# Kernel optimization log

Hardware: AMD Instinct MI355X
Metric: run time of the kernel (lower is better)

The kernel has to match this reference:

```python
import jax, jax.numpy as jnp
import numpy as np

B, S, I, H = 32, 1024, 512, 512


def setup_inputs() -> dict:
    key = jax.random.key(0)
    ks = jax.random.split(key, 5)
    scale_ih = 1.0 / np.sqrt(I)
    scale_hh = 1.0 / np.sqrt(H)
    return {
        "x": jax.random.normal(ks[0], (B, S, I), dtype=jnp.float32),
        "W_ih": jax.random.normal(ks[1], (4 * H, I), dtype=jnp.float32) * scale_ih,
        "W_hh": jax.random.normal(ks[2], (4 * H, H), dtype=jnp.float32) * scale_hh,
        "b_ih": jax.random.normal(ks[3], (4 * H,), dtype=jnp.float32) * scale_hh,
        "b_hh": jax.random.normal(ks[4], (4 * H,), dtype=jnp.float32) * scale_hh,
        "h0": jnp.zeros((B, H), dtype=jnp.float32),
        "c0": jnp.zeros((B, H), dtype=jnp.float32),
    }


def reference(x, W_ih, W_hh, b_ih, b_hh, h0, c0):
    # Precompute input contribution for all timesteps: [B, S, 4H]
    x_gates = jnp.einsum('bsi,gi->bsg', x, W_ih) + b_ih + b_hh

    def step(carry, xg_t):
        h, c = carry
        gates = xg_t + h @ W_hh.T  # [B, 4H]
        i_g, f_g, g_g, o_g = jnp.split(gates, 4, axis=-1)
        i_g = jax.nn.sigmoid(i_g)
        f_g = jax.nn.sigmoid(f_g)
        g_g = jnp.tanh(g_g)
        o_g = jax.nn.sigmoid(o_g)
        c_new = f_g * c + i_g * g_g
        h_new = o_g * jnp.tanh(c_new)
        return (h_new, c_new), h_new

    # scan over time: [S, B, 4H]
    (h_n, c_n), ys = jax.lax.scan(step, (h0, c0), jnp.swapaxes(x_gates, 0, 1))
    output = jnp.swapaxes(ys, 0, 1)  # [B, S, H]
    return output, h_n, c_n
```

## Files before the change

### kernel.cpp

```cpp
#include <hip/hip_runtime.h>
#include <stdint.h>


typedef __attribute__((ext_vector_type(8))) short bf16x8;
typedef __attribute__((ext_vector_type(4))) float f32x4;

__device__ __forceinline__ unsigned short f2bf(float f) {
  union { float f; unsigned u; } v; v.f = f;
  unsigned r = (v.u + 0x7fffu + ((v.u >> 16) & 1u)) >> 16;
  return (unsigned short)r;
}
__device__ __forceinline__ float bf2f(unsigned short h) {
  union { unsigned u; float f; } v; v.u = ((unsigned)h) << 16;
  return v.f;
}

__global__ __launch_bounds__(256) void cvt_bf16(const float* __restrict__ in,
                                                unsigned short* __restrict__ out, int n) {
  int i = (blockIdx.x * 256 + threadIdx.x) * 4;
  if (i >= n) return;
  float4 v = *(const float4*)(in + i);
  ushort4 o;
  o.x = f2bf(v.x); o.y = f2bf(v.y); o.z = f2bf(v.z); o.w = f2bf(v.w);
  *(ushort4*)(out + i) = o;
}

__global__ __launch_bounds__(256) void gemm_xg(const unsigned short* __restrict__ A,
                                               const unsigned short* __restrict__ Bw,
                                               const float* __restrict__ b_ih,
                                               const float* __restrict__ b_hh,
                                               unsigned short* __restrict__ xg) {
  __shared__ unsigned short Asub[128][32];
  __shared__ unsigned short Bsub[128][32];
  const int tid = threadIdx.x;
  const int mb = blockIdx.x >> 4;
  const int nb = blockIdx.x & 15;
  const int wv = tid >> 6, ln = tid & 63;
  const int wr = wv >> 1, wc = wv & 1;
  const int lrow = tid >> 1;
  const int lseg = (tid & 1) * 16;

  const unsigned short* Ag = A + (size_t)(mb * 128 + lrow) * 512 + lseg;
  const unsigned short* Bg = Bw + (size_t)(nb * 128 + lrow) * 512 + lseg;

  f32x4 acc[4][4] = {};
  const int frow = ln & 15;
  const int kq = (ln >> 4) * 8;

  for (int k0 = 0; k0 < 512; k0 += 32) {
    uint4 a0 = *(const uint4*)(Ag + k0);
    uint4 a1 = *(const uint4*)(Ag + k0 + 8);
    uint4 b0 = *(const uint4*)(Bg + k0);
    uint4 b1 = *(const uint4*)(Bg + k0 + 8);
    __syncthreads();
    *(uint4*)&Asub[lrow][lseg]     = a0;
    *(uint4*)&Asub[lrow][lseg + 8] = a1;
    *(uint4*)&Bsub[lrow][lseg]     = b0;
    *(uint4*)&Bsub[lrow][lseg + 8] = b1;
    __syncthreads();
    bf16x8 af[4], bfr[4];
#pragma unroll
    for (int mi = 0; mi < 4; ++mi)
      af[mi] = *(const bf16x8*)&Asub[wr * 64 + mi * 16 + frow][kq];
#pragma unroll
    for (int ni = 0; ni < 4; ++ni)
      bfr[ni] = *(const bf16x8*)&Bsub[wc * 64 + ni * 16 + frow][kq];
#pragma unroll
    for (int mi = 0; mi < 4; ++mi)
#pragma unroll
      for (int ni = 0; ni < 4; ++ni)
        acc[mi][ni] = __builtin_amdgcn_mfma_f32_16x16x32_bf16(af[mi], bfr[ni], acc[mi][ni], 0, 0, 0);
  }

  const int col0 = nb * 128 + wc * 64 + frow;
  float bias[4];
#pragma unroll
  for (int ni = 0; ni < 4; ++ni)
    bias[ni] = b_ih[col0 + ni * 16] + b_hh[col0 + ni * 16];

#pragma unroll
  for (int mi = 0; mi < 4; ++mi) {
    const int m0 = mb * 128 + wr * 64 + mi * 16 + (ln >> 4) * 4;
#pragma unroll
    for (int ni = 0; ni < 4; ++ni) {
#pragma unroll
      for (int rr = 0; rr < 4; ++rr) {
        float v = acc[mi][ni][rr] + bias[ni];
        xg[(size_t)(m0 + rr) * 2048 + col0 + ni * 16] = f2bf(v);
      }
    }
  }
}

__global__ __launch_bounds__(512, 1) void lstm_rec(const unsigned short* __restrict__ xg,
                                                   const float* __restrict__ W_hh,
                                                   const float* __restrict__ h0,
                                                   const float* __restrict__ c0,
                                                   float* __restrict__ out,
                                                   float* __restrict__ hn,
                                                   float* __restrict__ cn,
                                                   float* h_buf,
                                                   unsigned int* cnt) {
  __shared__ float h_lds[2048];
  __shared__ float scratch[2048];
  __shared__ float gates_lds[64 * 5];
  __shared__ float c_lds[64];

  const int tid = threadIdx.x;
  const int g = blockIdx.x >> 5;
  const int w = blockIdx.x & 31;
  const int gb0 = g * 4;
  const int kc = tid >> 6;
  const int r = tid & 63;
  const int grow = (r >> 4) * 512 + w * 16 + (r & 15);
  const int kcb = kc * 64;
  unsigned int* my_cnt = cnt + g * 64;

  float W[64];
  {
    const float* wp = W_hh + (size_t)grow * 512 + kcb;
#pragma unroll
    for (int i = 0; i < 64; i += 4) {
      float4 v = *(const float4*)(wp + i);
      W[i] = v.x; W[i + 1] = v.y; W[i + 2] = v.z; W[i + 3] = v.w;
    }
  }
#pragma unroll
  for (int i = 0; i < 64; ++i) asm volatile("" : "+v"(W[i]));

  {
    *(float4*)&h_lds[tid * 4] = *(const float4*)(h0 + gb0 * 512 + tid * 4);
    if (tid < 64) {
      int jj = tid & 15, bb = tid >> 4;
      c_lds[bb * 16 + jj] = c0[(gb0 + bb) * 512 + w * 16 + jj];
    }
  }
  __syncthreads();

  const int rr = tid & 63, bb2 = tid >> 6;
  const int grow_r = (rr >> 4) * 512 + w * 16 + (rr & 15);

  for (int t = 0; t < 1024; ++t) {
    float xg_v = 0.f;
    if (tid < 256)
      xg_v = bf2f(xg[(size_t)((gb0 + bb2) * 1024 + t) * 2048 + grow_r]);

    float acc0 = 0.f, acc1 = 0.f, acc2 = 0.f, acc3 = 0.f;
#pragma unroll
    for (int i = 0; i < 64; i += 4) {
      float4 ha = *(const float4*)&h_lds[kcb + i];
      float4 hb = *(const float4*)&h_lds[512 + kcb + i];
      float4 hc = *(const float4*)&h_lds[1024 + kcb + i];
      float4 hd = *(const float4*)&h_lds[1536 + kcb + i];
      acc0 = fmaf(W[i], ha.x, acc0); acc0 = fmaf(W[i + 1], ha.y, acc0);
      acc0 = fmaf(W[i + 2], ha.z, acc0); acc0 = fmaf(W[i + 3], ha.w, acc0);
      acc1 = fmaf(W[i], hb.x, acc1); acc1 = fmaf(W[i + 1], hb.y, acc1);
      acc1 = fmaf(W[i + 2], hb.z, acc1); acc1 = fmaf(W[i + 3], hb.w, acc1);
      acc2 = fmaf(W[i], hc.x, acc2); acc2 = fmaf(W[i + 1], hc.y, acc2);
      acc2 = fmaf(W[i + 2], hc.z, acc2); acc2 = fmaf(W[i + 3], hc.w, acc2);
      acc3 = fmaf(W[i], hd.x, acc3); acc3 = fmaf(W[i + 1], hd.y, acc3);
      acc3 = fmaf(W[i + 2], hd.z, acc3); acc3 = fmaf(W[i + 3], hd.w, acc3);
    }
    scratch[0 * 512 + kc * 64 + r] = acc0;
    scratch[1 * 512 + kc * 64 + r] = acc1;
    scratch[2 * 512 + kc * 64 + r] = acc2;
    scratch[3 * 512 + kc * 64 + r] = acc3;
    __syncthreads();

    if (tid < 256) {
      const float* sp = &scratch[bb2 * 512 + rr];
      float s = xg_v;
#pragma unroll
      for (int q = 0; q < 8; ++q) s += sp[q * 64];
      gates_lds[rr * 5 + bb2] = s;
    }
    __syncthreads();

    if (tid < 64) {
      const int jj = tid & 15, bb = tid >> 4;
      float gi = gates_lds[jj * 5 + bb];
      float gf = gates_lds[(16 + jj) * 5 + bb];
      float gc = gates_lds[(32 + jj) * 5 + bb];
      float go = gates_lds[(48 + jj) * 5 + bb];
      float ig = 1.f / (1.f + __expf(-gi));
      float fg = 1.f / (1.f + __expf(-gf));
      float gt = tanhf(gc);
      float og = 1.f / (1.f + __expf(-go));
      float c = fmaf(fg, c_lds[bb * 16 + jj], ig * gt);
      c_lds[bb * 16 + jj] = c;
      float hv = og * tanhf(c);
      out[(size_t)((gb0 + bb) * 1024 + t) * 512 + w * 16 + jj] = hv;
      __hip_atomic_store(&h_buf[((t + 1) & 1) * 16384 + (gb0 + bb) * 512 + w * 16 + jj], hv,
                         __ATOMIC_RELAXED, __HIP_MEMORY_SCOPE_AGENT);
      if (t == 1023) {
        hn[(gb0 + bb) * 512 + w * 16 + jj] = hv;
        cn[(gb0 + bb) * 512 + w * 16 + jj] = c;
      }
    }
    __syncthreads();

    if (t < 1023) {
      if (tid == 0) {
        __hip_atomic_fetch_add(my_cnt, 1u, __ATOMIC_RELAXED, __HIP_MEMORY_SCOPE_AGENT);
        const unsigned target = 32u * (unsigned)(t + 1);
        while (__hip_atomic_load(my_cnt, __ATOMIC_RELAXED, __HIP_MEMORY_SCOPE_AGENT) < target)
          __builtin_amdgcn_s_sleep(2);
      }
      __syncthreads();
      const unsigned long long* hb =
          (const unsigned long long*)(h_buf + ((t + 1) & 1) * 16384 + gb0 * 512 + tid * 4);
      unsigned long long v0 = __hip_atomic_load(hb,     __ATOMIC_RELAXED, __HIP_MEMORY_SCOPE_AGENT);
      unsigned long long v1 = __hip_atomic_load(hb + 1, __ATOMIC_RELAXED, __HIP_MEMORY_SCOPE_AGENT);
      *(unsigned long long*)&h_lds[tid * 4]     = v0;
      *(unsigned long long*)&h_lds[tid * 4 + 2] = v1;
      __syncthreads();
    }
  }
}

extern "C" void kernel_launch(void* const* d_in, const int* in_sizes, int n_in,
                              void* d_out, int out_size, void* d_ws, size_t ws_size,
                              hipStream_t stream) {
  const float* x    = (const float*)d_in[0];
  const float* W_ih = (const float*)d_in[1];
  const float* W_hh = (const float*)d_in[2];
  const float* b_ih = (const float*)d_in[3];
  const float* b_hh = (const float*)d_in[4];
  const float* h0   = (const float*)d_in[5];
  const float* c0   = (const float*)d_in[6];
  float* out = (float*)d_out;
  float* hn = out + (size_t)32 * 1024 * 512;
  float* cn = hn + 32 * 512;

  uint8_t* ws = (uint8_t*)d_ws;
  unsigned short* xg   = (unsigned short*)ws;
  unsigned short* x_bf = (unsigned short*)(ws + 134217728u);
  unsigned short* w_bf = (unsigned short*)(ws + 167772160u);
  float* h_buf         = (float*)(ws + 169869312u);
  unsigned int* cnt    = (unsigned int*)(ws + 170000384u);

  hipMemsetAsync(cnt, 0, 8 * 256, stream);
  cvt_bf16<<<dim3(16384), dim3(256), 0, stream>>>(x, x_bf, 16777216);
  cvt_bf16<<<dim3(1024), dim3(256), 0, stream>>>(W_ih, w_bf, 1048576);
  gemm_xg<<<dim3(4096), dim3(256), 0, stream>>>(x_bf, w_bf, b_ih, b_hh, xg);

  void* args[] = {(void*)&xg, (void*)&W_hh, (void*)&h0, (void*)&c0,
                  (void*)&out, (void*)&hn, (void*)&cn, (void*)&h_buf, (void*)&cnt};
  hipLaunchCooperativeKernel((const void*)lstm_rec, dim3(256), dim3(512), args, 0, stream);
}
```

Baseline: 3.388 ms.

## Retile recurrent matvec into 4x4 register blocks and fuse gate reduction via shuffles

Restructures the per-step W_hh·h product so each thread holds a 4-row by 16-column register tile of W and computes 4 rows times 4 batches. Each loaded h value is now reused across four weight rows. The cross-thread reduction writes padded scratch over 32 k-chunks, and the gate gather uses wave shuffles instead of a separate LDS gates buffer, which removes one __syncthreads per timestep. The block-to-(group, slice) mapping is also swapped so consecutive blocks belong to different batch groups. In exchange the reduction is longer (32 partials instead of 8) and scratch LDS grows.

```diff
diff --git a/kernel.cpp b/kernel.cpp
--- a/kernel.cpp
+++ b/kernel.cpp
@@ -92,6 +92,28 @@
   }
 }
 
+#define ROW_FMA(A, W0v, W1v, W2v, W3v)                                        \
+  A = fmaf(W0v.x, hv0.x, A); A = fmaf(W0v.y, hv0.y, A);                       \
+  A = fmaf(W0v.z, hv0.z, A); A = fmaf(W0v.w, hv0.w, A);                       \
+  A = fmaf(W1v.x, hv1.x, A); A = fmaf(W1v.y, hv1.y, A);                       \
+  A = fmaf(W1v.z, hv1.z, A); A = fmaf(W1v.w, hv1.w, A);                       \
+  A = fmaf(W2v.x, hv2.x, A); A = fmaf(W2v.y, hv2.y, A);                       \
+  A = fmaf(W2v.z, hv2.z, A); A = fmaf(W2v.w, hv2.w, A);                       \
+  A = fmaf(W3v.x, hv3.x, A); A = fmaf(W3v.y, hv3.y, A);                       \
+  A = fmaf(W3v.z, hv3.z, A); A = fmaf(W3v.w, hv3.w, A)
+
+#define FMA_BATCH(b)                                                          \
+  do {                                                                        \
+    f32x4 hv0 = *(const f32x4*)&h_lds[(b) * 512 + kcb16];                     \
+    f32x4 hv1 = *(const f32x4*)&h_lds[(b) * 512 + kcb16 + 4];                 \
+    f32x4 hv2 = *(const f32x4*)&h_lds[(b) * 512 + kcb16 + 8];                 \
+    f32x4 hv3 = *(const f32x4*)&h_lds[(b) * 512 + kcb16 + 12];                \
+    ROW_FMA(acc[0][b], Wr0_0, Wr0_1, Wr0_2, Wr0_3);                           \
+    ROW_FMA(acc[1][b], Wr1_0, Wr1_1, Wr1_2, Wr1_3);                           \
+    ROW_FMA(acc[2][b], Wr2_0, Wr2_1, Wr2_2, Wr2_3);                           \
+    ROW_FMA(acc[3][b], Wr3_0, Wr3_1, Wr3_2, Wr3_3);                           \
+  } while (0)
+
 __global__ __launch_bounds__(512, 1) void lstm_rec(const unsigned short* __restrict__ xg,
                                                    const float* __restrict__ W_hh,
                                                    const float* __restrict__ h0,
@@ -102,31 +124,35 @@
                                                    float* h_buf,
                                                    unsigned int* cnt) {
   __shared__ float h_lds[2048];
-  __shared__ float scratch[2048];
-  __shared__ float gates_lds[64 * 5];
+  __shared__ float scratch[8704];
   __shared__ float c_lds[64];
 
   const int tid = threadIdx.x;
-  const int g = blockIdx.x >> 5;
-  const int w = blockIdx.x & 31;
+  const int g = blockIdx.x & 7;
+  const int w = blockIdx.x >> 3;
   const int gb0 = g * 4;
-  const int kc = tid >> 6;
-  const int r = tid & 63;
-  const int grow = (r >> 4) * 512 + w * 16 + (r & 15);
-  const int kcb = kc * 64;
+  const int kc = tid >> 4;
+  const int rg = tid & 15;
+  const int kcb16 = kc * 16;
   unsigned int* my_cnt = cnt + g * 64;
 
-  float W[64];
-  {
-    const float* wp = W_hh + (size_t)grow * 512 + kcb;
-#pragma unroll
-    for (int i = 0; i < 64; i += 4) {
-      float4 v = *(const float4*)(wp + i);
-      W[i] = v.x; W[i + 1] = v.y; W[i + 2] = v.z; W[i + 3] = v.w;
-    }
-  }
-#pragma unroll
-  for (int i = 0; i < 64; ++i) asm volatile("" : "+v"(W[i]));
+  const int grow0 = (rg >> 2) * 512 + w * 16 + (rg & 3) * 4;
+  const float* wp0 = W_hh + (size_t)(grow0 + 0) * 512 + kcb16;
+  const float* wp1 = W_hh + (size_t)(grow0 + 1) * 512 + kcb16;
+  const float* wp2 = W_hh + (size_t)(grow0 + 2) * 512 + kcb16;
+  const float* wp3 = W_hh + (size_t)(grow0 + 3) * 512 + kcb16;
+  f32x4 Wr0_0 = *(const f32x4*)(wp0), Wr0_1 = *(const f32x4*)(wp0 + 4),
+        Wr0_2 = *(const f32x4*)(wp0 + 8), Wr0_3 = *(const f32x4*)(wp0 + 12);
+  f32x4 Wr1_0 = *(const f32x4*)(wp1), Wr1_1 = *(const f32x4*)(wp1 + 4),
+        Wr1_2 = *(const f32x4*)(wp1 + 8), Wr1_3 = *(const f32x4*)(wp1 + 12);
+  f32x4 Wr2_0 = *(const f32x4*)(wp2), Wr2_1 = *(const f32x4*)(wp2 + 4),
+        Wr2_2 = *(const f32x4*)(wp2 + 8), Wr2_3 = *(const f32x4*)(wp2 + 12);
+  f32x4 Wr3_0 = *(const f32x4*)(wp3), Wr3_1 = *(const f32x4*)(wp3 + 4),
+        Wr3_2 = *(const f32x4*)(wp3 + 8), Wr3_3 = *(const f32x4*)(wp3 + 12);
+  asm volatile("" : "+v"(Wr0_0), "+v"(Wr0_1), "+v"(Wr0_2), "+v"(Wr0_3),
+                    "+v"(Wr1_0), "+v"(Wr1_1), "+v"(Wr1_2), "+v"(Wr1_3),
+                    "+v"(Wr2_0), "+v"(Wr2_1), "+v"(Wr2_2), "+v"(Wr2_3),
+                    "+v"(Wr3_0), "+v"(Wr3_1), "+v"(Wr3_2), "+v"(Wr3_3));
 
   {
     *(float4*)&h_lds[tid * 4] = *(const float4*)(h0 + gb0 * 512 + tid * 4);
@@ -137,64 +163,57 @@
   }
   __syncthreads();
 
-  const int rr = tid & 63, bb2 = tid >> 6;
-  const int grow_r = (rr >> 4) * 512 + w * 16 + (rr & 15);
+  const int lane = tid & 63;
+  const int b2 = tid >> 6;
+  const int jj = lane & 15;
+  const int grow_r = (lane >> 4) * 512 + w * 16 + jj;
 
   for (int t = 0; t < 1024; ++t) {
     float xg_v = 0.f;
     if (tid < 256)
-      xg_v = bf2f(xg[(size_t)((gb0 + bb2) * 1024 + t) * 2048 + grow_r]);
-
-    float acc0 = 0.f, acc1 = 0.f, acc2 = 0.f, acc3 = 0.f;
-#pragma unroll
-    for (int i = 0; i < 64; i += 4) {
-      float4 ha = *(const float4*)&h_lds[kcb + i];
-      float4 hb = *(const float4*)&h_lds[512 + kcb + i];
-      float4 hc = *(const float4*)&h_lds[1024 + kcb + i];
-      float4 hd = *(const float4*)&h_lds[1536 + kcb + i];
-      acc0 = fmaf(W[i], ha.x, acc0); acc0 = fmaf(W[i + 1], ha.y, acc0);
-      acc0 = fmaf(W[i + 2], ha.z, acc0); acc0 = fmaf(W[i + 3], ha.w, acc0);
-      acc1 = fmaf(W[i], hb.x, acc1); acc1 = fmaf(W[i + 1], hb.y, acc1);
-      acc1 = fmaf(W[i + 2], hb.z, acc1); acc1 = fmaf(W[i + 3], hb.w, acc1);
-      acc2 = fmaf(W[i], hc.x, acc2); acc2 = fmaf(W[i + 1], hc.y, acc2);
-      acc2 = fmaf(W[i + 2], hc.z, acc2); acc2 = fmaf(W[i + 3], hc.w, acc2);
-      acc3 = fmaf(W[i], hd.x, acc3); acc3 = fmaf(W[i + 1], hd.y, acc3);
-      acc3 = fmaf(W[i + 2], hd.z, acc3); acc3 = fmaf(W[i + 3], hd.w, acc3);
-    }
-    scratch[0 * 512 + kc * 64 + r] = acc0;
-    scratch[1 * 512 + kc * 64 + r] = acc1;
-    scratch[2 * 512 + kc * 64 + r] = acc2;
-    scratch[3 * 512 + kc * 64 + r] = acc3;
+      xg_v = bf2f(xg[(size_t)((gb0 + b2) * 1024 + t) * 2048 + grow_r]);
+
+    float acc[4][4] = {};
+    FMA_BATCH(0); FMA_BATCH(1); FMA_BATCH(2); FMA_BATCH(3);
+
+#pragma unroll
+    for (int b = 0; b < 4; ++b) {
+      f32x4 v;
+      v.x = acc[0][b]; v.y = acc[1][b]; v.z = acc[2][b]; v.w = acc[3][b];
+      *(f32x4*)&scratch[b * 2176 + kc * 68 + rg * 4] = v;
+    }
     __syncthreads();
 
     if (tid < 256) {
-      const float* sp = &scratch[bb2 * 512 + rr];
-      float s = xg_v;
-#pragma unroll
-      for (int q = 0; q < 8; ++q) s += sp[q * 64];
-      gates_lds[rr * 5 + bb2] = s;
-    }
-    __syncthreads();
-
-    if (tid < 64) {
-      const int jj = tid & 15, bb = tid >> 4;
-      float gi = gates_lds[jj * 5 + bb];
-      float gf = gates_lds[(16 + jj) * 5 + bb];
-      float gc = gates_lds[(32 + jj) * 5 + bb];
-      float go = gates_lds[(48 + jj) * 5 + bb];
-      float ig = 1.f / (1.f + __expf(-gi));
-      float fg = 1.f / (1.f + __expf(-gf));
-      float gt = tanhf(gc);
-      float og = 1.f / (1.f + __expf(-go));
-      float c = fmaf(fg, c_lds[bb * 16 + jj], ig * gt);
-      c_lds[bb * 16 + jj] = c;
-      float hv = og * tanhf(c);
-      out[(size_t)((gb0 + bb) * 1024 + t) * 512 + w * 16 + jj] = hv;
-      __hip_atomic_store(&h_buf[((t + 1) & 1) * 16384 + (gb0 + bb) * 512 + w * 16 + jj], hv,
-                         __ATOMIC_RELAXED, __HIP_MEMORY_SCOPE_AGENT);
-      if (t == 1023) {
-        hn[(gb0 + bb) * 512 + w * 16 + jj] = hv;
-        cn[(gb0 + bb) * 512 + w * 16 + jj] = c;
+      const float* sp = &scratch[b2 * 2176 + lane];
+      float s0 = 0.f, s1 = 0.f, s2 = 0.f, s3 = 0.f;
+#pragma unroll
+      for (int q = 0; q < 32; q += 4) {
+        s0 += sp[q * 68];
+        s1 += sp[(q + 1) * 68];
+        s2 += sp[(q + 2) * 68];
+        s3 += sp[(q + 3) * 68];
+      }
+      float s = xg_v + ((s0 + s1) + (s2 + s3));
+      float gi = __shfl(s, jj);
+      float gf = __shfl(s, jj + 16);
+      float gc = __shfl(s, jj + 32);
+      float go = __shfl(s, jj + 48);
+      if (lane < 16) {
+        float ig = 1.f / (1.f + __expf(-gi));
+        float fg = 1.f / (1.f + __expf(-gf));
+        float gt = tanhf(gc);
+        float og = 1.f / (1.f + __expf(-go));
+        float c = fmaf(fg, c_lds[b2 * 16 + jj], ig * gt);
+        c_lds[b2 * 16 + jj] = c;
+        float hv = og * tanhf(c);
+        out[(size_t)((gb0 + b2) * 1024 + t) * 512 + w * 16 + jj] = hv;
+        __hip_atomic_store(&h_buf[((t + 1) & 1) * 16384 + (gb0 + b2) * 512 + w * 16 + jj], hv,
+                           __ATOMIC_RELAXED, __HIP_MEMORY_SCOPE_AGENT);
+        if (t == 1023) {
+          hn[(gb0 + b2) * 512 + w * 16 + jj] = hv;
+          cn[(gb0 + b2) * 512 + w * 16 + jj] = c;
+        }
       }
     }
     __syncthreads();
```

Measured after the change: 3.220 ms. 4.9% less time.
